# Performance work log

Measured on AMD Instinct MI355X. Metric: run time of the kernel, lower is better.

## Reference

```python
import jax, jax.numpy as jnp
import numpy as np

N_NODES = 100000
N_EDGES = 3200000
NODE_DIM = 128
HIDDEN = 16


def setup_inputs() -> dict:
    key = jax.random.key(0)
    ks = jax.random.split(key, 12)
    x = jax.random.normal(ks[0], (N_NODES, NODE_DIM), dtype=jnp.float32)
    edge_src = jax.random.randint(ks[1], (N_EDGES,), 0, N_NODES, dtype=jnp.int32)
    edge_dst = jax.random.randint(ks[2], (N_EDGES,), 0, N_NODES, dtype=jnp.int32)
    # QCNN block params (Linear(node_dim,16), Linear(16,16), Linear(16,16)) + classifier Linear(16,1)
    s1 = 1.0 / np.sqrt(NODE_DIM)
    s2 = 1.0 / np.sqrt(HIDDEN)
    W1 = jax.random.uniform(ks[3], (NODE_DIM, HIDDEN), jnp.float32, -s1, s1)
    b1 = jax.random.uniform(ks[4], (HIDDEN,), jnp.float32, -s1, s1)
    W2 = jax.random.uniform(ks[5], (HIDDEN, HIDDEN), jnp.float32, -s2, s2)
    b2 = jax.random.uniform(ks[6], (HIDDEN,), jnp.float32, -s2, s2)
    W3 = jax.random.uniform(ks[7], (HIDDEN, HIDDEN), jnp.float32, -s2, s2)
    b3 = jax.random.uniform(ks[8], (HIDDEN,), jnp.float32, -s2, s2)
    Wc = jax.random.uniform(ks[9], (HIDDEN, 1), jnp.float32, -s2, s2)
    bc = jax.random.uniform(ks[10], (1,), jnp.float32, -s2, s2)
    return {"x": x, "edge_src": edge_src, "edge_dst": edge_dst,
            "W1": W1, "b1": b1, "W2": W2, "b2": b2, "W3": W3, "b3": b3,
            "Wc": Wc, "bc": bc}


def reference(x, edge_src, edge_dst, W1, b1, W2, b2, W3, b3, Wc, bc):
    # per-node tiny 3-layer tanh MLP (QCNN block), vectorized over all nodes
    h = jnp.tanh(x @ W1 + b1)
    h = jnp.tanh(h @ W2 + b2)
    h = jnp.tanh(h @ W3 + b3)  # [N, H]
    n = x.shape[0]
    # degree of each aggregating node; nodes with no neighbors contribute 0
    deg = jnp.zeros((n,), x.dtype).at[edge_src].add(1.0)
    inv_deg = jnp.where(deg > 0, 1.0 / jnp.maximum(deg, 1.0), 0.0)
    # aggregated = sum_n mean_{m in N(n)} h[m] = sum_e h[dst_e] / deg[src_e]
    agg = jnp.sum(h[edge_dst] * inv_deg[edge_src][:, None], axis=0) / n  # [H]
    return jax.nn.sigmoid(agg @ Wc + bc)  # [1]
```

## Files before the change

### kernel.cpp

```cpp
#include <hip/hip_runtime.h>
#include <math.h>


#define NODE_DIM 128
#define HID 16

typedef __attribute__((ext_vector_type(8))) short    bfrag8;
typedef __attribute__((ext_vector_type(4))) _Float16 hfrag4;
typedef __attribute__((ext_vector_type(4))) float    f32x4;

__device__ __forceinline__ float fast_tanh(float x) {
    x = fminf(fmaxf(x, -10.0f), 10.0f);
    float e = __expf(2.0f * x);
    return (e - 1.0f) * __frcp_rn(e + 1.0f);
}
__device__ __forceinline__ unsigned short f2bf(float f) {
    unsigned u = __float_as_uint(f);
    return (unsigned short)((u + 0x7FFFu + ((u >> 16) & 1u)) >> 16);
}

__global__ __launch_bounds__(256) void k_mlp(
    const float* __restrict__ x,
    const float* __restrict__ W1, const float* __restrict__ b1,
    const float* __restrict__ W2, const float* __restrict__ b2,
    const float* __restrict__ W3, const float* __restrict__ b3,
    const float* __restrict__ Wc,
    unsigned char* __restrict__ c_code, int n_nodes)
{
    const int lane = threadIdx.x & 63;
    const int col  = lane & 15;
    const int q    = lane >> 4;

    bfrag8 w1f[4];
#pragma unroll
    for (int kc = 0; kc < 4; ++kc)
#pragma unroll
        for (int j = 0; j < 8; ++j)
            w1f[kc][j] = (short)f2bf(W1[(kc * 32 + q * 8 + j) * HID + col]);

    hfrag4 w2t, w3t;
#pragma unroll
    for (int j = 0; j < 4; ++j) {
        w2t[j] = (_Float16)W2[(q * 4 + j) * HID + col];
        w3t[j] = (_Float16)W3[(q * 4 + j) * HID + col];
    }
    float bb1[4], bb2[4], bb3[4], wcr[4];
#pragma unroll
    for (int j = 0; j < 4; ++j) {
        bb1[j] = b1[q * 4 + j]; bb2[j] = b2[q * 4 + j];
        bb3[j] = b3[q * 4 + j]; wcr[j] = Wc[q * 4 + j];
    }

    const int ngroups = (n_nodes + 15) >> 4;
    const int nwaves  = gridDim.x * (blockDim.x >> 6);
    const int wgid    = (blockIdx.x * blockDim.x + threadIdx.x) >> 6;
    const f32x4 zero = {0.f, 0.f, 0.f, 0.f};

    for (int g = wgid; g < ngroups; g += nwaves) {
        const int node0 = g << 4;
        int m = node0 + col;
        int mload = (m < n_nodes) ? m : (n_nodes - 1);
        const float* xr = x + (size_t)mload * NODE_DIM;

        float4 xa[4], xb[4];
#pragma unroll
        for (int kc = 0; kc < 4; ++kc) {
            const float* p = xr + kc * 32 + q * 8;
            xa[kc] = *reinterpret_cast<const float4*>(p);
            xb[kc] = *reinterpret_cast<const float4*>(p + 4);
        }
        f32x4 d1 = zero;
#pragma unroll
        for (int kc = 0; kc < 4; ++kc) {
            bfrag8 bf;
            bf[0] = (short)f2bf(xa[kc].x); bf[1] = (short)f2bf(xa[kc].y);
            bf[2] = (short)f2bf(xa[kc].z); bf[3] = (short)f2bf(xa[kc].w);
            bf[4] = (short)f2bf(xb[kc].x); bf[5] = (short)f2bf(xb[kc].y);
            bf[6] = (short)f2bf(xb[kc].z); bf[7] = (short)f2bf(xb[kc].w);
            d1 = __builtin_amdgcn_mfma_f32_16x16x32_bf16(w1f[kc], bf, d1, 0, 0, 0);
        }
        hfrag4 h1;
#pragma unroll
        for (int r = 0; r < 4; ++r) h1[r] = (_Float16)fast_tanh(d1[r] + bb1[r]);

        f32x4 d2 = __builtin_amdgcn_mfma_f32_16x16x16f16(w2t, h1, zero, 0, 0, 0);
        hfrag4 h2;
#pragma unroll
        for (int r = 0; r < 4; ++r) h2[r] = (_Float16)fast_tanh(d2[r] + bb2[r]);

        f32x4 d3 = __builtin_amdgcn_mfma_f32_16x16x16f16(w3t, h2, zero, 0, 0, 0);

        float v = 0.0f;
#pragma unroll
        for (int r = 0; r < 4; ++r) v += fast_tanh(d3[r] + bb3[r]) * wcr[r];
        v += __shfl_xor(v, 16, 64);
        v += __shfl_xor(v, 32, 64);

        if (lane < 16) {
            const int node = node0 + lane;
            if (node < n_nodes) {
                float c = fminf(fmaxf(v, -4.0f), 4.0f);
                c_code[node] = (unsigned char)__float2int_rn((c + 4.0f) * 16.0f);
            }
        }
    }
}

__global__ __launch_bounds__(1024) void k_gather(
    const int* __restrict__ dst, const unsigned char* __restrict__ c_code,
    unsigned char* __restrict__ rec, int n_edges, int ch, int n_chunks, int n_slices)
{
    extern __shared__ unsigned char dynlds[];
    unsigned char* sc = dynlds;
    const int tid   = threadIdx.x;
    const int chunk = blockIdx.x % n_chunks;
    const int slice = blockIdx.x / n_chunks;
    const int lo    = chunk * ch;

    const unsigned int* cp = reinterpret_cast<const unsigned int*>(c_code);
    unsigned int* scp = reinterpret_cast<unsigned int*>(sc);
    for (int i = tid; i < (ch >> 2); i += 1024)
        scp[i] = cp[(size_t)chunk * (ch >> 2) + i];
    __syncthreads();

    if (n_chunks == 1) {
        const int epb = ((n_edges + n_slices - 1) / n_slices + 7) & ~7;
        const int e0 = slice * epb;
        const int e1 = min(e0 + epb, n_edges);
        for (int e = e0 + (tid << 3); e < e1; e += 1024 * 8) {
            if (e + 7 < e1) {
                int4 d0 = *reinterpret_cast<const int4*>(dst + e);
                int4 d1 = *reinterpret_cast<const int4*>(dst + e + 4);
                uint2 r;
                r.x = (unsigned)sc[d0.x] | ((unsigned)sc[d0.y] << 8)
                    | ((unsigned)sc[d0.z] << 16) | ((unsigned)sc[d0.w] << 24);
                r.y = (unsigned)sc[d1.x] | ((unsigned)sc[d1.y] << 8)
                    | ((unsigned)sc[d1.z] << 16) | ((unsigned)sc[d1.w] << 24);
                *reinterpret_cast<uint2*>(rec + e) = r;
            } else {
                for (int j = e; j < e1; ++j) rec[j] = sc[dst[j]];
            }
        }
    } else {
        const int epb = ((n_edges + n_slices - 1) / n_slices + 3) & ~3;
        const int e0 = slice * epb;
        const int e1 = min(e0 + epb, n_edges);
        for (int e = e0 + (tid << 2); e < e1; e += 1024 * 4) {
            if (e + 3 < e1) {
                int4 d = *reinterpret_cast<const int4*>(dst + e);
                if ((unsigned)(d.x - lo) < (unsigned)ch) rec[e + 0] = sc[d.x - lo];
                if ((unsigned)(d.y - lo) < (unsigned)ch) rec[e + 1] = sc[d.y - lo];
                if ((unsigned)(d.z - lo) < (unsigned)ch) rec[e + 2] = sc[d.z - lo];
                if ((unsigned)(d.w - lo) < (unsigned)ch) rec[e + 3] = sc[d.w - lo];
            } else {
                for (int j = e; j < e1; ++j) {
                    int dd = dst[j];
                    if ((unsigned)(dd - lo) < (unsigned)ch) rec[j] = sc[dd - lo];
                }
            }
        }
    }
}

__global__ __launch_bounds__(1024) void k_accum(
    const int* __restrict__ src, const unsigned char* __restrict__ rec,
    unsigned int* __restrict__ tables, int n_edges, int ch, int n_chunks, int n_slices)
{
    extern __shared__ unsigned char dynlds[];
    unsigned int* tab = (unsigned int*)dynlds;
    const int tid   = threadIdx.x;
    const int chunk = blockIdx.x % n_chunks;
    const int slice = blockIdx.x / n_chunks;
    const int lo    = chunk * ch;
    const int words = ch >> 1;

    uint4* t4 = reinterpret_cast<uint4*>(tab);
    const uint4 z4 = {0u, 0u, 0u, 0u};
    for (int i = tid; i < (words >> 2); i += 1024) t4[i] = z4;
    __syncthreads();

    const int epb = ((n_edges + n_slices - 1) / n_slices + 7) & ~7;
    const int e0 = slice * epb;
    const int e1 = min(e0 + epb, n_edges);

    for (int e = e0 + (tid << 3); e < e1; e += 1024 * 8) {
        if (e + 7 < e1) {
            int4 s0 = *reinterpret_cast<const int4*>(src + e);
            int4 s1 = *reinterpret_cast<const int4*>(src + e + 4);
            uchar4 r0 = *reinterpret_cast<const uchar4*>(rec + e);
            uchar4 r1 = *reinterpret_cast<const uchar4*>(rec + e + 4);
            int i0 = s0.x - lo, i1 = s0.y - lo, i2 = s0.z - lo, i3 = s0.w - lo;
            int i4 = s1.x - lo, i5 = s1.y - lo, i6 = s1.z - lo, i7 = s1.w - lo;
            if ((unsigned)i0 < (unsigned)ch) atomicAdd(&tab[i0 >> 1], ((1u << 12) | (unsigned)r0.x) << ((i0 & 1) << 4));
            if ((unsigned)i1 < (unsigned)ch) atomicAdd(&tab[i1 >> 1], ((1u << 12) | (unsigned)r0.y) << ((i1 & 1) << 4));
            if ((unsigned)i2 < (unsigned)ch) atomicAdd(&tab[i2 >> 1], ((1u << 12) | (unsigned)r0.z) << ((i2 & 1) << 4));
            if ((unsigned)i3 < (unsigned)ch) atomicAdd(&tab[i3 >> 1], ((1u << 12) | (unsigned)r0.w) << ((i3 & 1) << 4));
            if ((unsigned)i4 < (unsigned)ch) atomicAdd(&tab[i4 >> 1], ((1u << 12) | (unsigned)r1.x) << ((i4 & 1) << 4));
            if ((unsigned)i5 < (unsigned)ch) atomicAdd(&tab[i5 >> 1], ((1u << 12) | (unsigned)r1.y) << ((i5 & 1) << 4));
            if ((unsigned)i6 < (unsigned)ch) atomicAdd(&tab[i6 >> 1], ((1u << 12) | (unsigned)r1.z) << ((i6 & 1) << 4));
            if ((unsigned)i7 < (unsigned)ch) atomicAdd(&tab[i7 >> 1], ((1u << 12) | (unsigned)r1.w) << ((i7 & 1) << 4));
        } else {
            for (int j = e; j < e1; ++j) {
                int ss = src[j] - lo;
                if ((unsigned)ss < (unsigned)ch)
                    atomicAdd(&tab[ss >> 1], ((1u << 12) | (unsigned)rec[j]) << ((ss & 1) << 4));
            }
        }
    }
    __syncthreads();
    uint4* out4 = reinterpret_cast<uint4*>(tables + (size_t)(slice * n_chunks + chunk) * words);
    for (int i = tid; i < (words >> 2); i += 1024) out4[i] = t4[i];
}

__global__ __launch_bounds__(256) void k_total(
    const unsigned int* __restrict__ tables, float* __restrict__ partials,
    int n_chunks, int ch, int n_slices)
{
    __shared__ float swave[4];
    const int wpc = ch >> 1;
    const int wg  = blockIdx.x * blockDim.x + threadIdx.x;
    const int chunk = wg / wpc, w = wg - chunk * wpc;
    const unsigned int stride = (unsigned int)(n_chunks * wpc);
    const unsigned int base0  = (unsigned int)(chunk * wpc + w);

    unsigned int sfix = 0, scnt = 0;
    for (int s = 0; s < n_slices; s += 8) {
        unsigned int v[8];
#pragma unroll
        for (int k = 0; k < 8; ++k)
            v[k] = tables[(size_t)(s + k) * stride + base0];
#pragma unroll
        for (int k = 0; k < 8; ++k) {
            sfix += v[k] & 0x0FFF0FFFu;
            scnt += (v[k] >> 12) & 0x000F000Fu;
        }
    }
    const unsigned int cnt_lo = scnt & 0xFFFFu, cnt_hi = scnt >> 16;
    const unsigned int fix_lo = sfix & 0xFFFFu, fix_hi = sfix >> 16;
    float contrib = 0.0f;
    if (cnt_lo > 0) contrib += (float)fix_lo / (16.0f * (float)cnt_lo) - 4.0f;
    if (cnt_hi > 0) contrib += (float)fix_hi / (16.0f * (float)cnt_hi) - 4.0f;

    for (int off = 32; off > 0; off >>= 1) contrib += __shfl_down(contrib, off, 64);
    if ((threadIdx.x & 63) == 0) swave[threadIdx.x >> 6] = contrib;
    __syncthreads();
    if (threadIdx.x == 0)
        partials[blockIdx.x] = swave[0] + swave[1] + swave[2] + swave[3];
}

__global__ __launch_bounds__(256) void k_final(
    const float* __restrict__ partials, const float* __restrict__ bc,
    float* __restrict__ out, float inv_n, int n_partials)
{
    __shared__ float swave[4];
    float v = (threadIdx.x < n_partials) ? partials[threadIdx.x] : 0.0f;
    for (int off = 32; off > 0; off >>= 1) v += __shfl_down(v, off, 64);
    if ((threadIdx.x & 63) == 0) swave[threadIdx.x >> 6] = v;
    __syncthreads();
    if (threadIdx.x == 0) {
        float sv = (swave[0] + swave[1] + swave[2] + swave[3]) * inv_n + bc[0];
        out[0] = 1.0f / (1.0f + __expf(-sv));
    }
}

extern "C" void kernel_launch(void* const* d_in, const int* in_sizes, int n_in,
                              void* d_out, int out_size, void* d_ws, size_t ws_size,
                              hipStream_t stream) {
    const float* x   = (const float*)d_in[0];
    const int* esrc  = (const int*)d_in[1];
    const int* edst  = (const int*)d_in[2];
    const float* W1  = (const float*)d_in[3];
    const float* b1  = (const float*)d_in[4];
    const float* W2  = (const float*)d_in[5];
    const float* b2  = (const float*)d_in[6];
    const float* W3  = (const float*)d_in[7];
    const float* b3  = (const float*)d_in[8];
    const float* Wc  = (const float*)d_in[9];
    const float* bc  = (const float*)d_in[10];

    const int n_nodes = in_sizes[0] / NODE_DIM;
    const int n_edges = in_sizes[1];
    const int ne_pad  = (n_edges + 15) & ~15;

    bool big = true;
    if (hipFuncSetAttribute((const void*)k_gather,
            hipFuncAttributeMaxDynamicSharedMemorySize, 131072) != hipSuccess) big = false;
    if (hipFuncSetAttribute((const void*)k_accum,
            hipFuncAttributeMaxDynamicSharedMemorySize, 131072) != hipSuccess) big = false;

    const int ch_g  = big ? ((n_nodes + 1023) & ~1023) : 51200;
    const int nch_g = (n_nodes + ch_g - 1) / ch_g;
    const int ch_a  = big ? 65536 : 32768;
    const int nch_a = (n_nodes + ch_a - 1) / ch_a;
    const int nsl   = 128;

    const size_t tab_b = (size_t)nsl * nch_a * ch_a * 2;
    unsigned int* tables = (unsigned int*)d_ws;
    float* partials = (float*)((char*)d_ws + tab_b);
    unsigned char* rec    = (unsigned char*)((char*)partials + 256 * sizeof(float));
    unsigned char* c_code = rec + ne_pad;

    k_mlp<<<512, 256, 0, stream>>>(x, W1, b1, W2, b2, W3, b3, Wc, c_code, n_nodes);

    const int nsl_g = 256 / nch_g;
    k_gather<<<nch_g * nsl_g, 1024, (size_t)ch_g, stream>>>(
        edst, c_code, rec, n_edges, ch_g, nch_g, nsl_g);

    k_accum<<<nch_a * nsl, 1024, (size_t)ch_a * 2, stream>>>(
        esrc, rec, tables, n_edges, ch_a, nch_a, nsl);

    const int nwords = (nch_a * ch_a) >> 1;
    const int ntb = nwords / 256;
    k_total<<<ntb, 256, 0, stream>>>(tables, partials, nch_a, ch_a, nsl);
    k_final<<<1, 256, 0, stream>>>(partials, bc, (float*)d_out,
                                   1.0f / (float)n_nodes, ntb);
}
```

Baseline: 142.9 us.

## Precompute node degrees, then replace per-node atomic tables with a direct weighted dot product

Adds a separate degree pass: per-slice LDS histograms with packed 4-bit counters, reduced into 8-bit per-node degrees. The aggregation kernel then loads the degrees into LDS and sums code/deg directly per edge into a float partial. This removes the large per-slice fix/count tables and the k_total pass that read them back, cutting global memory traffic and LDS atomics in the aggregation. The trade-offs are a second read of the src array, two extra launches, and a degree cap of 255. It also makes the MLP grid size depend on the node count.

Result: slower. 155.7 us (+9.0%).

```diff
diff --git a/kernel.cpp b/kernel.cpp
--- a/kernel.cpp
+++ b/kernel.cpp
@@ -104,6 +104,78 @@
             }
         }
     }
+}
+
+__global__ __launch_bounds__(1024) void k_deg(
+    const int* __restrict__ src, unsigned int* __restrict__ dtab,
+    int n_edges, int words, int n_slices)
+{
+    extern __shared__ unsigned char dynlds[];
+    unsigned int* tab = (unsigned int*)dynlds;
+    const int tid   = threadIdx.x;
+    const int slice = blockIdx.x;
+
+    uint4* t4 = reinterpret_cast<uint4*>(tab);
+    const uint4 z4 = {0u, 0u, 0u, 0u};
+    for (int i = tid; i < (words >> 2); i += 1024) t4[i] = z4;
+    __syncthreads();
+
+    const int epb = ((n_edges + n_slices - 1) / n_slices + 7) & ~7;
+    const int e0 = slice * epb;
+    const int e1 = min(e0 + epb, n_edges);
+
+    for (int e = e0 + (tid << 3); e < e1; e += 1024 * 8) {
+        if (e + 7 < e1) {
+            int4 s0 = *reinterpret_cast<const int4*>(src + e);
+            int4 s1 = *reinterpret_cast<const int4*>(src + e + 4);
+            atomicAdd(&tab[s0.x >> 3], 1u << ((s0.x & 7) << 2));
+            atomicAdd(&tab[s0.y >> 3], 1u << ((s0.y & 7) << 2));
+            atomicAdd(&tab[s0.z >> 3], 1u << ((s0.z & 7) << 2));
+            atomicAdd(&tab[s0.w >> 3], 1u << ((s0.w & 7) << 2));
+            atomicAdd(&tab[s1.x >> 3], 1u << ((s1.x & 7) << 2));
+            atomicAdd(&tab[s1.y >> 3], 1u << ((s1.y & 7) << 2));
+            atomicAdd(&tab[s1.z >> 3], 1u << ((s1.z & 7) << 2));
+            atomicAdd(&tab[s1.w >> 3], 1u << ((s1.w & 7) << 2));
+        } else {
+            for (int j = e; j < e1; ++j) {
+                int ss = src[j];
+                atomicAdd(&tab[ss >> 3], 1u << ((ss & 7) << 2));
+            }
+        }
+    }
+    __syncthreads();
+    uint4* out4 = reinterpret_cast<uint4*>(dtab + (size_t)slice * words);
+    for (int i = tid; i < (words >> 2); i += 1024) out4[i] = t4[i];
+}
+
+__global__ __launch_bounds__(256) void k_degsum(
+    const unsigned int* __restrict__ dtab, unsigned char* __restrict__ deg8,
+    int words, int n_slices)
+{
+    const int i = blockIdx.x * 256 + threadIdx.x;
+    if (i >= words) return;
+    unsigned int a0 = 0, a1 = 0, a2 = 0, a3 = 0;
+    for (int sg = 0; sg < n_slices; sg += 16) {
+        unsigned int lo = 0, hi = 0;
+#pragma unroll
+        for (int k = 0; k < 16; ++k) {
+            unsigned int w = dtab[(size_t)(sg + k) * words + i];
+            lo += w & 0x0F0F0F0Fu;
+            hi += (w >> 4) & 0x0F0F0F0Fu;
+        }
+        a0 += lo & 0x00FF00FFu;
+        a1 += (lo >> 8) & 0x00FF00FFu;
+        a2 += hi & 0x00FF00FFu;
+        a3 += (hi >> 8) & 0x00FF00FFu;
+    }
+    unsigned int d0 = min(a0 & 0xFFFFu, 255u), d1 = min(a2 & 0xFFFFu, 255u);
+    unsigned int d2 = min(a1 & 0xFFFFu, 255u), d3 = min(a3 & 0xFFFFu, 255u);
+    unsigned int d4 = min(a0 >> 16, 255u),     d5 = min(a2 >> 16, 255u);
+    unsigned int d6 = min(a1 >> 16, 255u),     d7 = min(a3 >> 16, 255u);
+    uint2 o;
+    o.x = d0 | (d1 << 8) | (d2 << 16) | (d3 << 24);
+    o.y = d4 | (d5 << 8) | (d6 << 16) | (d7 << 24);
+    *reinterpret_cast<uint2*>(deg8 + (size_t)i * 8) = o;
 }
 
 __global__ __launch_bounds__(1024) void k_gather(
@@ -162,90 +234,72 @@
     }
 }
 
-__global__ __launch_bounds__(1024) void k_accum(
+__global__ __launch_bounds__(1024) void k_dot(
     const int* __restrict__ src, const unsigned char* __restrict__ rec,
-    unsigned int* __restrict__ tables, int n_edges, int ch, int n_chunks, int n_slices)
+    const unsigned char* __restrict__ deg8, float* __restrict__ partials,
+    int n_edges, int ch, int n_chunks, int n_slices)
 {
     extern __shared__ unsigned char dynlds[];
-    unsigned int* tab = (unsigned int*)dynlds;
+    unsigned char* sd = dynlds;
+    __shared__ float swave[16];
     const int tid   = threadIdx.x;
     const int chunk = blockIdx.x % n_chunks;
     const int slice = blockIdx.x / n_chunks;
     const int lo    = chunk * ch;
-    const int words = ch >> 1;
-
-    uint4* t4 = reinterpret_cast<uint4*>(tab);
-    const uint4 z4 = {0u, 0u, 0u, 0u};
-    for (int i = tid; i < (words >> 2); i += 1024) t4[i] = z4;
-    __syncthreads();
-
+
+    const unsigned int* dp = reinterpret_cast<const unsigned int*>(deg8);
+    unsigned int* sdp = reinterpret_cast<unsigned int*>(sd);
+    for (int i = tid; i < (ch >> 2); i += 1024)
+        sdp[i] = dp[(size_t)chunk * (ch >> 2) + i];
+    __syncthreads();
+
+    float acc = 0.0f;
     const int epb = ((n_edges + n_slices - 1) / n_slices + 7) & ~7;
     const int e0 = slice * epb;
     const int e1 = min(e0 + epb, n_edges);
 
-    for (int e = e0 + (tid << 3); e < e1; e += 1024 * 8) {
-        if (e + 7 < e1) {
-            int4 s0 = *reinterpret_cast<const int4*>(src + e);
-            int4 s1 = *reinterpret_cast<const int4*>(src + e + 4);
-            uchar4 r0 = *reinterpret_cast<const uchar4*>(rec + e);
-            uchar4 r1 = *reinterpret_cast<const uchar4*>(rec + e + 4);
-            int i0 = s0.x - lo, i1 = s0.y - lo, i2 = s0.z - lo, i3 = s0.w - lo;
-            int i4 = s1.x - lo, i5 = s1.y - lo, i6 = s1.z - lo, i7 = s1.w - lo;
-            if ((unsigned)i0 < (unsigned)ch) atomicAdd(&tab[i0 >> 1], ((1u << 12) | (unsigned)r0.x) << ((i0 & 1) << 4));
-            if ((unsigned)i1 < (unsigned)ch) atomicAdd(&tab[i1 >> 1], ((1u << 12) | (unsigned)r0.y) << ((i1 & 1) << 4));
-            if ((unsigned)i2 < (unsigned)ch) atomicAdd(&tab[i2 >> 1], ((1u << 12) | (unsigned)r0.z) << ((i2 & 1) << 4));
-            if ((unsigned)i3 < (unsigned)ch) atomicAdd(&tab[i3 >> 1], ((1u << 12) | (unsigned)r0.w) << ((i3 & 1) << 4));
-            if ((unsigned)i4 < (unsigned)ch) atomicAdd(&tab[i4 >> 1], ((1u << 12) | (unsigned)r1.x) << ((i4 & 1) << 4));
-            if ((unsigned)i5 < (unsigned)ch) atomicAdd(&tab[i5 >> 1], ((1u << 12) | (unsigned)r1.y) << ((i5 & 1) << 4));
-            if ((unsigned)i6 < (unsigned)ch) atomicAdd(&tab[i6 >> 1], ((1u << 12) | (unsigned)r1.z) << ((i6 & 1) << 4));
-            if ((unsigned)i7 < (unsigned)ch) atomicAdd(&tab[i7 >> 1], ((1u << 12) | (unsigned)r1.w) << ((i7 & 1) << 4));
-        } else {
-            for (int j = e; j < e1; ++j) {
+#define EDGE1(S, CODE) { unsigned int dd_ = sd[S];                              \
+        float iv_ = dd_ ? __frcp_rn(16.0f * (float)dd_) : 0.0f;                 \
+        acc += (float)((int)(CODE) - 64) * iv_; }
+
+    if (n_chunks == 1) {
+        for (int e = e0 + (tid << 3); e < e1; e += 1024 * 8) {
+            if (e + 7 < e1) {
+                int4 s0 = *reinterpret_cast<const int4*>(src + e);
+                int4 s1 = *reinterpret_cast<const int4*>(src + e + 4);
+                uint2 r = *reinterpret_cast<const uint2*>(rec + e);
+                EDGE1(s0.x,  r.x        & 0xFFu);
+                EDGE1(s0.y, (r.x >>  8) & 0xFFu);
+                EDGE1(s0.z, (r.x >> 16) & 0xFFu);
+                EDGE1(s0.w, (r.x >> 24) & 0xFFu);
+                EDGE1(s1.x,  r.y        & 0xFFu);
+                EDGE1(s1.y, (r.y >>  8) & 0xFFu);
+                EDGE1(s1.z, (r.y >> 16) & 0xFFu);
+                EDGE1(s1.w, (r.y >> 24) & 0xFFu);
+            } else {
+                for (int j = e; j < e1; ++j) EDGE1(src[j], rec[j]);
+            }
+        }
+    } else {
+        for (int e = e0 + (tid << 3); e < e1; e += 1024 * 8) {
+            int ee = min(e + 8, e1);
+            for (int j = e; j < ee; ++j) {
                 int ss = src[j] - lo;
-                if ((unsigned)ss < (unsigned)ch)
-                    atomicAdd(&tab[ss >> 1], ((1u << 12) | (unsigned)rec[j]) << ((ss & 1) << 4));
-            }
-        }
-    }
-    __syncthreads();
-    uint4* out4 = reinterpret_cast<uint4*>(tables + (size_t)(slice * n_chunks + chunk) * words);
-    for (int i = tid; i < (words >> 2); i += 1024) out4[i] = t4[i];
-}
-
-__global__ __launch_bounds__(256) void k_total(
-    const unsigned int* __restrict__ tables, float* __restrict__ partials,
-    int n_chunks, int ch, int n_slices)
-{
-    __shared__ float swave[4];
-    const int wpc = ch >> 1;
-    const int wg  = blockIdx.x * blockDim.x + threadIdx.x;
-    const int chunk = wg / wpc, w = wg - chunk * wpc;
-    const unsigned int stride = (unsigned int)(n_chunks * wpc);
-    const unsigned int base0  = (unsigned int)(chunk * wpc + w);
-
-    unsigned int sfix = 0, scnt = 0;
-    for (int s = 0; s < n_slices; s += 8) {
-        unsigned int v[8];
-#pragma unroll
-        for (int k = 0; k < 8; ++k)
-            v[k] = tables[(size_t)(s + k) * stride + base0];
-#pragma unroll
-        for (int k = 0; k < 8; ++k) {
-            sfix += v[k] & 0x0FFF0FFFu;
-            scnt += (v[k] >> 12) & 0x000F000Fu;
-        }
-    }
-    const unsigned int cnt_lo = scnt & 0xFFFFu, cnt_hi = scnt >> 16;
-    const unsigned int fix_lo = sfix & 0xFFFFu, fix_hi = sfix >> 16;
-    float contrib = 0.0f;
-    if (cnt_lo > 0) contrib += (float)fix_lo / (16.0f * (float)cnt_lo) - 4.0f;
-    if (cnt_hi > 0) contrib += (float)fix_hi / (16.0f * (float)cnt_hi) - 4.0f;
-
-    for (int off = 32; off > 0; off >>= 1) contrib += __shfl_down(contrib, off, 64);
-    if ((threadIdx.x & 63) == 0) swave[threadIdx.x >> 6] = contrib;
-    __syncthreads();
-    if (threadIdx.x == 0)
-        partials[blockIdx.x] = swave[0] + swave[1] + swave[2] + swave[3];
+                if ((unsigned)ss < (unsigned)ch) EDGE1(ss, rec[j]);
+            }
+        }
+    }
+#undef EDGE1
+
+    for (int off = 32; off > 0; off >>= 1) acc += __shfl_down(acc, off, 64);
+    if ((tid & 63) == 0) swave[tid >> 6] = acc;
+    __syncthreads();
+    if (tid == 0) {
+        float s = 0.0f;
+#pragma unroll
+        for (int w = 0; w < 16; ++w) s += swave[w];
+        partials[blockIdx.x] = s;
+    }
 }
 
 __global__ __launch_bounds__(256) void k_final(
@@ -285,33 +339,41 @@
     bool big = true;
     if (hipFuncSetAttribute((const void*)k_gather,
             hipFuncAttributeMaxDynamicSharedMemorySize, 131072) != hipSuccess) big = false;
-    if (hipFuncSetAttribute((const void*)k_accum,
+    if (hipFuncSetAttribute((const void*)k_dot,
             hipFuncAttributeMaxDynamicSharedMemorySize, 131072) != hipSuccess) big = false;
+
+    int words = (n_nodes + 7) >> 3;
+    words = (words + 3) & ~3;
+    const int nsl_d = 128;
 
     const int ch_g  = big ? ((n_nodes + 1023) & ~1023) : 51200;
     const int nch_g = (n_nodes + ch_g - 1) / ch_g;
-    const int ch_a  = big ? 65536 : 32768;
-    const int nch_a = (n_nodes + ch_a - 1) / ch_a;
-    const int nsl   = 128;
-
-    const size_t tab_b = (size_t)nsl * nch_a * ch_a * 2;
-    unsigned int* tables = (unsigned int*)d_ws;
-    float* partials = (float*)((char*)d_ws + tab_b);
-    unsigned char* rec    = (unsigned char*)((char*)partials + 256 * sizeof(float));
+    const int ch_t  = big ? ((n_nodes + 1023) & ~1023) : 51200;
+    const int nch_t = (n_nodes + ch_t - 1) / ch_t;
+
+    const size_t dtab_b = (size_t)nsl_d * words * 4;
+    unsigned int* dtab    = (unsigned int*)d_ws;
+    float* partials       = (float*)((char*)d_ws + dtab_b);
+    unsigned char* rec    = (unsigned char*)partials + 256 * sizeof(float);
     unsigned char* c_code = rec + ne_pad;
-
-    k_mlp<<<512, 256, 0, stream>>>(x, W1, b1, W2, b2, W3, b3, Wc, c_code, n_nodes);
+    unsigned char* deg8   = c_code + (size_t)nch_g * ch_g;
+
+    const int ngroups  = (n_nodes + 15) >> 4;
+    const int mlp_grid = min(1024, (ngroups + 3) >> 2);
+    k_mlp<<<mlp_grid, 256, 0, stream>>>(x, W1, b1, W2, b2, W3, b3, Wc, c_code, n_nodes);
+
+    k_deg<<<nsl_d, 1024, (size_t)words * 4, stream>>>(esrc, dtab, n_edges, words, nsl_d);
+
+    k_degsum<<<(words + 255) >> 8, 256, 0, stream>>>(dtab, deg8, words, nsl_d);
 
     const int nsl_g = 256 / nch_g;
     k_gather<<<nch_g * nsl_g, 1024, (size_t)ch_g, stream>>>(
         edst, c_code, rec, n_edges, ch_g, nch_g, nsl_g);
 
-    k_accum<<<nch_a * nsl, 1024, (size_t)ch_a * 2, stream>>>(
-        esrc, rec, tables, n_edges, ch_a, nch_a, nsl);
-
-    const int nwords = (nch_a * ch_a) >> 1;
-    const int ntb = nwords / 256;
-    k_total<<<ntb, 256, 0, stream>>>(tables, partials, nch_a, ch_a, nsl);
+    const int nsl_t = 256 / nch_t;
+    k_dot<<<nch_t * nsl_t, 1024, (size_t)ch_t, stream>>>(
+        esrc, rec, deg8, partials, n_edges, ch_t, nch_t, nsl_t);
+
     k_final<<<1, 256, 0, stream>>>(partials, bc, (float*)d_out,
-                                   1.0f / (float)n_nodes, ntb);
-}
+                                   1.0f / (float)n_nodes, nch_t * nsl_t);
+}
```

## Fuse gather into accumulation and merge total/final reductions via ticket

Applied to the files above, without the earlier changes.

Removes the separate gather kernel and its per-edge byte buffer: the accumulation kernel now looks up each destination's code directly from global memory (L2-resident 100KB table) instead of via an LDS-staged copy and an intermediate rec array. The total and final reduction kernels are merged using a global atomic float sum with a last-block ticket. Chunk size changes to 50176 so two chunks cover the nodes. This trades a pass over the edge list and two launches for random global byte loads inside the atomic loop, and duplicates dst reads across the two chunks.

After: 152.6 us. 6.8% more time.

```diff
diff --git a/kernel.cpp b/kernel.cpp
--- a/kernel.cpp
+++ b/kernel.cpp
@@ -106,65 +106,12 @@
     }
 }
 
-__global__ __launch_bounds__(1024) void k_gather(
-    const int* __restrict__ dst, const unsigned char* __restrict__ c_code,
-    unsigned char* __restrict__ rec, int n_edges, int ch, int n_chunks, int n_slices)
-{
-    extern __shared__ unsigned char dynlds[];
-    unsigned char* sc = dynlds;
-    const int tid   = threadIdx.x;
-    const int chunk = blockIdx.x % n_chunks;
-    const int slice = blockIdx.x / n_chunks;
-    const int lo    = chunk * ch;
-
-    const unsigned int* cp = reinterpret_cast<const unsigned int*>(c_code);
-    unsigned int* scp = reinterpret_cast<unsigned int*>(sc);
-    for (int i = tid; i < (ch >> 2); i += 1024)
-        scp[i] = cp[(size_t)chunk * (ch >> 2) + i];
-    __syncthreads();
-
-    if (n_chunks == 1) {
-        const int epb = ((n_edges + n_slices - 1) / n_slices + 7) & ~7;
-        const int e0 = slice * epb;
-        const int e1 = min(e0 + epb, n_edges);
-        for (int e = e0 + (tid << 3); e < e1; e += 1024 * 8) {
-            if (e + 7 < e1) {
-                int4 d0 = *reinterpret_cast<const int4*>(dst + e);
-                int4 d1 = *reinterpret_cast<const int4*>(dst + e + 4);
-                uint2 r;
-                r.x = (unsigned)sc[d0.x] | ((unsigned)sc[d0.y] << 8)
-                    | ((unsigned)sc[d0.z] << 16) | ((unsigned)sc[d0.w] << 24);
-                r.y = (unsigned)sc[d1.x] | ((unsigned)sc[d1.y] << 8)
-                    | ((unsigned)sc[d1.z] << 16) | ((unsigned)sc[d1.w] << 24);
-                *reinterpret_cast<uint2*>(rec + e) = r;
-            } else {
-                for (int j = e; j < e1; ++j) rec[j] = sc[dst[j]];
-            }
-        }
-    } else {
-        const int epb = ((n_edges + n_slices - 1) / n_slices + 3) & ~3;
-        const int e0 = slice * epb;
-        const int e1 = min(e0 + epb, n_edges);
-        for (int e = e0 + (tid << 2); e < e1; e += 1024 * 4) {
-            if (e + 3 < e1) {
-                int4 d = *reinterpret_cast<const int4*>(dst + e);
-                if ((unsigned)(d.x - lo) < (unsigned)ch) rec[e + 0] = sc[d.x - lo];
-                if ((unsigned)(d.y - lo) < (unsigned)ch) rec[e + 1] = sc[d.y - lo];
-                if ((unsigned)(d.z - lo) < (unsigned)ch) rec[e + 2] = sc[d.z - lo];
-                if ((unsigned)(d.w - lo) < (unsigned)ch) rec[e + 3] = sc[d.w - lo];
-            } else {
-                for (int j = e; j < e1; ++j) {
-                    int dd = dst[j];
-                    if ((unsigned)(dd - lo) < (unsigned)ch) rec[j] = sc[dd - lo];
-                }
-            }
-        }
-    }
-}
-
-__global__ __launch_bounds__(1024) void k_accum(
-    const int* __restrict__ src, const unsigned char* __restrict__ rec,
-    unsigned int* __restrict__ tables, int n_edges, int ch, int n_chunks, int n_slices)
+__global__ __launch_bounds__(1024) void k_gaccum(
+    const int* __restrict__ src, const int* __restrict__ dst,
+    const unsigned char* __restrict__ c_code,
+    unsigned int* __restrict__ tables,
+    float* __restrict__ gtotal, unsigned int* __restrict__ ticket,
+    int n_edges, int ch, int n_chunks, int n_slices)
 {
     extern __shared__ unsigned char dynlds[];
     unsigned int* tab = (unsigned int*)dynlds;
@@ -174,6 +121,8 @@
     const int lo    = chunk * ch;
     const int words = ch >> 1;
 
+    if (blockIdx.x == 0 && tid == 0) { *gtotal = 0.0f; *ticket = 0u; }
+
     uint4* t4 = reinterpret_cast<uint4*>(tab);
     const uint4 z4 = {0u, 0u, 0u, 0u};
     for (int i = tid; i < (words >> 2); i += 1024) t4[i] = z4;
@@ -187,23 +136,28 @@
         if (e + 7 < e1) {
             int4 s0 = *reinterpret_cast<const int4*>(src + e);
             int4 s1 = *reinterpret_cast<const int4*>(src + e + 4);
-            uchar4 r0 = *reinterpret_cast<const uchar4*>(rec + e);
-            uchar4 r1 = *reinterpret_cast<const uchar4*>(rec + e + 4);
+            int4 d0 = *reinterpret_cast<const int4*>(dst + e);
+            int4 d1 = *reinterpret_cast<const int4*>(dst + e + 4);
+            unsigned c0 = c_code[d0.x], c1 = c_code[d0.y];
+            unsigned c2 = c_code[d0.z], c3 = c_code[d0.w];
+            unsigned c4 = c_code[d1.x], c5 = c_code[d1.y];
+            unsigned c6 = c_code[d1.z], c7 = c_code[d1.w];
             int i0 = s0.x - lo, i1 = s0.y - lo, i2 = s0.z - lo, i3 = s0.w - lo;
             int i4 = s1.x - lo, i5 = s1.y - lo, i6 = s1.z - lo, i7 = s1.w - lo;
-            if ((unsigned)i0 < (unsigned)ch) atomicAdd(&tab[i0 >> 1], ((1u << 12) | (unsigned)r0.x) << ((i0 & 1) << 4));
-            if ((unsigned)i1 < (unsigned)ch) atomicAdd(&tab[i1 >> 1], ((1u << 12) | (unsigned)r0.y) << ((i1 & 1) << 4));
-            if ((unsigned)i2 < (unsigned)ch) atomicAdd(&tab[i2 >> 1], ((1u << 12) | (unsigned)r0.z) << ((i2 & 1) << 4));
-            if ((unsigned)i3 < (unsigned)ch) atomicAdd(&tab[i3 >> 1], ((1u << 12) | (unsigned)r0.w) << ((i3 & 1) << 4));
-            if ((unsigned)i4 < (unsigned)ch) atomicAdd(&tab[i4 >> 1], ((1u << 12) | (unsigned)r1.x) << ((i4 & 1) << 4));
-            if ((unsigned)i5 < (unsigned)ch) atomicAdd(&tab[i5 >> 1], ((1u << 12) | (unsigned)r1.y) << ((i5 & 1) << 4));
-            if ((unsigned)i6 < (unsigned)ch) atomicAdd(&tab[i6 >> 1], ((1u << 12) | (unsigned)r1.z) << ((i6 & 1) << 4));
-            if ((unsigned)i7 < (unsigned)ch) atomicAdd(&tab[i7 >> 1], ((1u << 12) | (unsigned)r1.w) << ((i7 & 1) << 4));
+            if ((unsigned)i0 < (unsigned)ch) atomicAdd(&tab[i0 >> 1], ((1u << 12) | c0) << ((i0 & 1) << 4));
+            if ((unsigned)i1 < (unsigned)ch) atomicAdd(&tab[i1 >> 1], ((1u << 12) | c1) << ((i1 & 1) << 4));
+            if ((unsigned)i2 < (unsigned)ch) atomicAdd(&tab[i2 >> 1], ((1u << 12) | c2) << ((i2 & 1) << 4));
+            if ((unsigned)i3 < (unsigned)ch) atomicAdd(&tab[i3 >> 1], ((1u << 12) | c3) << ((i3 & 1) << 4));
+            if ((unsigned)i4 < (unsigned)ch) atomicAdd(&tab[i4 >> 1], ((1u << 12) | c4) << ((i4 & 1) << 4));
+            if ((unsigned)i5 < (unsigned)ch) atomicAdd(&tab[i5 >> 1], ((1u << 12) | c5) << ((i5 & 1) << 4));
+            if ((unsigned)i6 < (unsigned)ch) atomicAdd(&tab[i6 >> 1], ((1u << 12) | c6) << ((i6 & 1) << 4));
+            if ((unsigned)i7 < (unsigned)ch) atomicAdd(&tab[i7 >> 1], ((1u << 12) | c7) << ((i7 & 1) << 4));
         } else {
             for (int j = e; j < e1; ++j) {
                 int ss = src[j] - lo;
                 if ((unsigned)ss < (unsigned)ch)
-                    atomicAdd(&tab[ss >> 1], ((1u << 12) | (unsigned)rec[j]) << ((ss & 1) << 4));
+                    atomicAdd(&tab[ss >> 1],
+                              ((1u << 12) | (unsigned)c_code[dst[j]]) << ((ss & 1) << 4));
             }
         }
     }
@@ -212,9 +166,11 @@
     for (int i = tid; i < (words >> 2); i += 1024) out4[i] = t4[i];
 }
 
-__global__ __launch_bounds__(256) void k_total(
-    const unsigned int* __restrict__ tables, float* __restrict__ partials,
-    int n_chunks, int ch, int n_slices)
+__global__ __launch_bounds__(256) void k_totalfinal(
+    const unsigned int* __restrict__ tables, const float* __restrict__ bc,
+    float* __restrict__ out, float* __restrict__ gtotal,
+    unsigned int* __restrict__ ticket,
+    int n_chunks, int ch, int n_slices, float inv_n, int ntb)
 {
     __shared__ float swave[4];
     const int wpc = ch >> 1;
@@ -244,22 +200,17 @@
     for (int off = 32; off > 0; off >>= 1) contrib += __shfl_down(contrib, off, 64);
     if ((threadIdx.x & 63) == 0) swave[threadIdx.x >> 6] = contrib;
     __syncthreads();
-    if (threadIdx.x == 0)
-        partials[blockIdx.x] = swave[0] + swave[1] + swave[2] + swave[3];
-}
-
-__global__ __launch_bounds__(256) void k_final(
-    const float* __restrict__ partials, const float* __restrict__ bc,
-    float* __restrict__ out, float inv_n, int n_partials)
-{
-    __shared__ float swave[4];
-    float v = (threadIdx.x < n_partials) ? partials[threadIdx.x] : 0.0f;
-    for (int off = 32; off > 0; off >>= 1) v += __shfl_down(v, off, 64);
-    if ((threadIdx.x & 63) == 0) swave[threadIdx.x >> 6] = v;
-    __syncthreads();
     if (threadIdx.x == 0) {
-        float sv = (swave[0] + swave[1] + swave[2] + swave[3]) * inv_n + bc[0];
-        out[0] = 1.0f / (1.0f + __expf(-sv));
+        float part = swave[0] + swave[1] + swave[2] + swave[3];
+        atomicAdd(gtotal, part);
+        __threadfence();
+        unsigned int t = atomicAdd(ticket, 1u);
+        if (t == (unsigned int)(ntb - 1)) {
+            __threadfence();
+            float tot = atomicAdd(gtotal, 0.0f);
+            float sv = tot * inv_n + bc[0];
+            out[0] = 1.0f / (1.0f + __expf(-sv));
+        }
     }
 }
 
@@ -280,38 +231,29 @@
 
     const int n_nodes = in_sizes[0] / NODE_DIM;
     const int n_edges = in_sizes[1];
-    const int ne_pad  = (n_edges + 15) & ~15;
 
     bool big = true;
-    if (hipFuncSetAttribute((const void*)k_gather,
+    if (hipFuncSetAttribute((const void*)k_gaccum,
             hipFuncAttributeMaxDynamicSharedMemorySize, 131072) != hipSuccess) big = false;
-    if (hipFuncSetAttribute((const void*)k_accum,
-            hipFuncAttributeMaxDynamicSharedMemorySize, 131072) != hipSuccess) big = false;
-
-    const int ch_g  = big ? ((n_nodes + 1023) & ~1023) : 51200;
-    const int nch_g = (n_nodes + ch_g - 1) / ch_g;
-    const int ch_a  = big ? 65536 : 32768;
+
+    const int ch_a  = big ? 50176 : 32768;
     const int nch_a = (n_nodes + ch_a - 1) / ch_a;
     const int nsl   = 128;
-
-    const size_t tab_b = (size_t)nsl * nch_a * ch_a * 2;
-    unsigned int* tables = (unsigned int*)d_ws;
-    float* partials = (float*)((char*)d_ws + tab_b);
-    unsigned char* rec    = (unsigned char*)((char*)partials + 256 * sizeof(float));
-    unsigned char* c_code = rec + ne_pad;
+    const int words = ch_a >> 1;
+
+    const size_t tab_b = (size_t)nsl * nch_a * words * 4;
+    unsigned int* tables  = (unsigned int*)d_ws;
+    float* gtotal         = (float*)((char*)d_ws + tab_b);
+    unsigned int* ticket  = (unsigned int*)(gtotal + 1);
+    unsigned char* c_code = (unsigned char*)d_ws + tab_b + 16;
 
     k_mlp<<<512, 256, 0, stream>>>(x, W1, b1, W2, b2, W3, b3, Wc, c_code, n_nodes);
 
-    const int nsl_g = 256 / nch_g;
-    k_gather<<<nch_g * nsl_g, 1024, (size_t)ch_g, stream>>>(
-        edst, c_code, rec, n_edges, ch_g, nch_g, nsl_g);
-
-    k_accum<<<nch_a * nsl, 1024, (size_t)ch_a * 2, stream>>>(
-        esrc, rec, tables, n_edges, ch_a, nch_a, nsl);
-
-    const int nwords = (nch_a * ch_a) >> 1;
-    const int ntb = nwords / 256;
-    k_total<<<ntb, 256, 0, stream>>>(tables, partials, nch_a, ch_a, nsl);
-    k_final<<<1, 256, 0, stream>>>(partials, bc, (float*)d_out,
-                                   1.0f / (float)n_nodes, ntb);
-}
+    k_gaccum<<<nsl * nch_a, 1024, (size_t)ch_a * 2, stream>>>(
+        esrc, edst, c_code, tables, gtotal, ticket, n_edges, ch_a, nch_a, nsl);
+
+    const int ntb = (nch_a * words) / 256;
+    k_totalfinal<<<ntb, 256, 0, stream>>>(
+        tables, bc, (float*)d_out, gtotal, ticket,
+        nch_a, ch_a, nsl, 1.0f / (float)n_nodes, ntb);
+}
```
